# Optimization experiments

Measured on AMD Instinct MI355X. Metric: run time of the kernel, lower is better.

## Reference

```python
import jax, jax.numpy as jnp
import numpy as np
from functools import partial

T, B, I, H, L = 512, 256, 12, 256, 3


def setup_inputs() -> dict:
    key = jax.random.key(0)
    ks = jax.random.split(key, 1 + 4 * L + 2)
    inp = {"input": jax.random.normal(ks[0], (T, B, I), dtype=jnp.float32)}
    k = 1
    for l in range(L):
        in_dim = I if l == 0 else H
        s = 1.0 / np.sqrt(H)
        inp[f"w_ih{l}"] = jax.random.uniform(ks[k], (4 * H, in_dim), jnp.float32, -s, s); k += 1
        inp[f"w_hh{l}"] = jax.random.uniform(ks[k], (4 * H, H), jnp.float32, -s, s); k += 1
        inp[f"b_ih{l}"] = jax.random.uniform(ks[k], (4 * H,), jnp.float32, -s, s); k += 1
        inp[f"b_hh{l}"] = jax.random.uniform(ks[k], (4 * H,), jnp.float32, -s, s); k += 1
    s = 1.0 / np.sqrt(H)
    inp["w_lin"] = jax.random.uniform(ks[k], (1, H), jnp.float32, -s, s); k += 1
    inp["b_lin"] = jax.random.uniform(ks[k], (1,), jnp.float32, -s, s)
    return inp


def _lstm_layer(x, w_ih, w_hh, b_ih, b_hh):
    # x: (T, B, in_dim) -> hidden sequence (T, B, H)
    h_dim = w_hh.shape[1]
    xproj = jnp.einsum('tbi,gi->tbg', x, w_ih) + b_ih + b_hh  # (T, B, 4H)

    def step(carry, xp):
        h, c = carry
        gates = xp + h @ w_hh.T  # (B, 4H), torch gate order i,f,g,o
        i, f, g, o = jnp.split(gates, 4, axis=-1)
        i = jax.nn.sigmoid(i); f = jax.nn.sigmoid(f)
        g = jnp.tanh(g); o = jax.nn.sigmoid(o)
        c = f * c + i * g
        h = o * jnp.tanh(c)
        return (h, c), h

    bsz = x.shape[1]
    h0 = jnp.zeros((bsz, h_dim), x.dtype)
    c0 = jnp.zeros((bsz, h_dim), x.dtype)
    _, hs = jax.lax.scan(step, (h0, c0), xproj)
    return hs


def reference(input, w_ih0, w_hh0, b_ih0, b_hh0, w_ih1, w_hh1, b_ih1, b_hh1,
              w_ih2, w_hh2, b_ih2, b_hh2, w_lin, b_lin):
    params = [(w_ih0, w_hh0, b_ih0, b_hh0),
              (w_ih1, w_hh1, b_ih1, b_hh1),
              (w_ih2, w_hh2, b_ih2, b_hh2)]
    h = input
    for w_ih, w_hh, b_ih, b_hh in params:
        h = _lstm_layer(h, w_ih, w_hh, b_ih, b_hh)
    out = h @ w_lin.T + b_lin  # (T, B, 1)
    return out[..., 0]  # matches torch stack+squeeze -> (T, B)
```

## Files before the change

kernel.cpp:

```cpp
#include <hip/hip_runtime.h>

typedef _Float16 f16;
typedef _Float16 f16x4 __attribute__((ext_vector_type(4)));
typedef _Float16 f16x8 __attribute__((ext_vector_type(8)));
typedef float f32x4 __attribute__((ext_vector_type(4)));
typedef unsigned long long u64;

#define NSTEPS 512
#define NBATCH 256
#define HID 256
#define NL 3
#define NBG 8
#define NNW 8
#define ROWS 32
#define DRING 8
#define PITCH 260
#define THREADS 256
#define BKB 15
#define FLAGSTRIDE 16
#define NEG_INF_I (-2000000000)

#define WPACK_OFF ((size_t)65536)
#define WPACK_ELEMS ((size_t)64*16*64*8)
#define WPACK_SZB (WPACK_ELEMS*2)
#define RING_OFF (WPACK_OFF + 3*WPACK_SZB)
#define SLOT_Q 2048
#define RING_SZB ((size_t)NL*NBG*DRING*SLOT_Q*8)
#define WS_NEEDED (RING_OFF + RING_SZB)

__device__ __forceinline__ float sigm(float x){ return 1.f/(1.f+__expf(-x)); }
__device__ __forceinline__ float tanh_f(float x){ return 1.f - 2.f/(1.f+__expf(2.f*x)); }

__global__ __launch_bounds__(256) void pack_weights(
    const float* __restrict__ wih0, const float* __restrict__ whh0,
    const float* __restrict__ wih1, const float* __restrict__ whh1,
    const float* __restrict__ wih2, const float* __restrict__ whh2,
    unsigned char* __restrict__ ws)
{
  int gid = blockIdx.x*256 + threadIdx.x;
  if (gid >= 3*64*16*64) return;
  int lane  = gid & 63;
  int kb    = (gid>>6) & 15;
  int nt    = (gid>>10) & 63;
  int layer = gid>>16;
  const float* whh = (layer==0)?whh0:((layer==1)?whh1:whh2);
  const float* wih = (layer==0)?wih0:((layer==1)?wih1:wih2);
  int indim = (layer==0)?12:256;
  int n  = nt*16 + (lane&15);
  int k0 = kb*32 + (lane>>4)*8;
  f16x8 v;
  #pragma unroll
  for (int e=0;e<8;++e){
    int k = k0+e;
    float x;
    if (k < HID) x = whh[n*HID + k];
    else { int ki = k-HID; x = (ki<indim)? wih[n*indim+ki] : 0.f; }
    v[e] = (f16)x;
  }
  f16* dst = (f16*)(ws + WPACK_OFF) + (size_t)layer*WPACK_ELEMS
           + ((size_t)(nt*16+kb)*64 + lane)*8;
  *(f16x8*)dst = v;
}

template<int KB>
__device__ __forceinline__ void gates_mfma(
    const f16* __restrict__ Hown, const f16* __restrict__ Hin,
    const f16* __restrict__ BstL, const f16x8* __restrict__ b15,
    const float* __restrict__ bias,
    int wm, int wn, int lane, int c16, f32x4* acc)
{
  const int arow = wm*16 + c16;
  #pragma unroll
  for (int G=0;G<4;++G){ f32x4 z={bias[G],bias[G],bias[G],bias[G]}; acc[G]=z; }
  #pragma unroll
  for (int kb=0; kb<KB; ++kb){
    const f16* ap = (kb<8) ? &Hown[arow*PITCH + kb*32 + (lane>>4)*8]
                           : &Hin [arow*PITCH + (kb-8)*32 + (lane>>4)*8];
    f16x8 a = *(const f16x8*)ap;
    #pragma unroll
    for (int G=0; G<4; ++G){
      f16x8 b = (kb < BKB)
        ? ((const f16x8*)BstL)[ (size_t)((G*2+wn)*BKB + kb)*64 + lane ]
        : b15[G];
      acc[G] = __builtin_amdgcn_mfma_f32_16x16x32_f16(a, b, acc[G], 0,0,0);
    }
  }
}

__global__ __launch_bounds__(THREADS) void lstm_ws(
    const float* __restrict__ input,
    const float* __restrict__ bih0, const float* __restrict__ bhh0,
    const float* __restrict__ bih1, const float* __restrict__ bhh1,
    const float* __restrict__ bih2, const float* __restrict__ bhh2,
    const float* __restrict__ wlin, const float* __restrict__ blin,
    unsigned char* __restrict__ ws, float* __restrict__ out)
{
  __shared__ __attribute__((aligned(16))) f16 Bst[8*BKB*64*8];
  __shared__ __attribute__((aligned(16))) f16 Hown[ROWS*PITCH];
  __shared__ __attribute__((aligned(16))) f16 Hin [ROWS*PITCH];
  __shared__ float wlinLDS[HID];

  const int tid  = threadIdx.x;
  const int w    = tid >> 6;
  const int wm   = w >> 1, wn = w & 1;
  const int lane = tid & 63;
  const int c16  = lane & 15;
  const int r0   = (lane >> 4) * 4;
  const int bid  = blockIdx.x;
  const int bg   = bid & 7;
  const int nw   = (bid >> 3) & 7;
  const int layer= bid >> 6;
  const int rowsBase = bg * ROWS;
  const int unitBase = nw * 32;

  int* flags = (int*)ws;
  int* fOwn  = flags + (layer*NBG + bg)*32*FLAGSTRIDE;
  int* fLow  = (layer>0)? flags + ((layer-1)*NBG + bg)*32*FLAGSTRIDE : fOwn;
  int* fUp   = (layer<2)? flags + ((layer+1)*NBG + bg)*32*FLAGSTRIDE : fOwn;

  const f16* wp = (const f16*)(ws + WPACK_OFF) + (size_t)layer*WPACK_ELEMS;
  u64* ringSelfQ = (u64*)(ws + RING_OFF) + (size_t)((layer*NBG + bg)*DRING)*SLOT_Q;
  u64* ringLowQ  = (layer>0)? (u64*)(ws + RING_OFF) + (size_t)(((layer-1)*NBG + bg)*DRING)*SLOT_Q : (u64*)0;

  const f16x8* wpv = (const f16x8*)wp;
  f16x8* Bv = (f16x8*)Bst;
  #pragma unroll
  for (int nl=0; nl<8; ++nl){
    int G = nl>>1, s = nl&1;
    int nt = G*16 + nw*2 + s;
    for (int idx=tid; idx<BKB*64; idx+=THREADS)
      Bv[(size_t)nl*BKB*64 + idx] = wpv[(size_t)nt*1024 + idx];
  }
  f16x8 b15[4];
  #pragma unroll
  for (int G=0; G<4; ++G){
    int nt = G*16 + nw*2 + wn;
    b15[G] = wpv[(size_t)nt*1024 + 15*64 + lane];
  }
  if (tid < HID) wlinLDS[tid] = wlin[tid];

  const float* BIH = (layer==0)?bih0:((layer==1)?bih1:bih2);
  const float* BHH = (layer==0)?bhh0:((layer==1)?bhh1:bhh2);
  float bias[4], cst[4];
  const int unit = unitBase + wn*16 + c16;
  #pragma unroll
  for (int G=0;G<4;++G){
    int n = G*HID + unit;
    bias[G] = BIH[n] + BHH[n];
    cst[G] = 0.f;
  }
  const float bl = blin[0];
  const int rowblk = wm*4 + (r0>>2);

  for (int i=tid; i<ROWS*PITCH; i+=THREADS){ Hown[i]=(f16)0.f; Hin[i]=(f16)0.f; }
  __syncthreads();

  for (int t=0; t<NSTEPS; ++t){
    {
      const int which = lane >> 5, fidx = lane & 31;
      bool act = (which==0) || (layer>0);
      const int* p = (which==0)? fOwn + fidx*FLAGSTRIDE : fLow + fidx*FLAGSTRIDE;
      int need = act ? ((which==0)? t : t+1) : NEG_INF_I;
      int guard = 0;
      for(;;){
        int v = act ? __hip_atomic_load(p, __ATOMIC_RELAXED, __HIP_MEMORY_SCOPE_AGENT) : 0;
        if (__all(v >= need)) break;
        if (++guard > (1<<22)) break;
      }
    }
    if (layer<2 && (t&3)==0 && t>4){
      bool act = lane < 32;
      const int* p = fUp + (lane&31)*FLAGSTRIDE;
      int need = act ? t-4 : NEG_INF_I;
      int guard = 0;
      for(;;){
        int v = act ? __hip_atomic_load(p, __ATOMIC_RELAXED, __HIP_MEMORY_SCOPE_AGENT) : 0;
        if (__all(v >= need)) break;
        if (++guard > (1<<22)) break;
      }
    }
    asm volatile("" ::: "memory");

    u64 vown[8], vin[8];
    if (t > 0){
      const u64* src = ringSelfQ + (size_t)((t-1)&(DRING-1))*SLOT_Q;
      #pragma unroll
      for (int it=0; it<8; ++it)
        vown[it] = __hip_atomic_load(src + tid + it*THREADS,
                                     __ATOMIC_RELAXED, __HIP_MEMORY_SCOPE_AGENT);
    }
    if (layer > 0){
      const u64* src = ringLowQ + (size_t)(t&(DRING-1))*SLOT_Q;
      #pragma unroll
      for (int it=0; it<8; ++it)
        vin[it] = __hip_atomic_load(src + tid + it*THREADS,
                                    __ATOMIC_RELAXED, __HIP_MEMORY_SCOPE_AGENT);
    }
    if (t > 0){
      #pragma unroll
      for (int it=0; it<8; ++it){
        int i = tid + it*THREADS, rb = i>>8, un = i&255;
        union { u64 q; f16x4 h; } u; u.q = vown[it];
        f16* base = &Hown[(rb*4)*PITCH + un];
        base[0]=u.h[0]; base[PITCH]=u.h[1]; base[2*PITCH]=u.h[2]; base[3*PITCH]=u.h[3];
      }
    }
    if (layer > 0){
      #pragma unroll
      for (int it=0; it<8; ++it){
        int i = tid + it*THREADS, rb = i>>8, un = i&255;
        union { u64 q; f16x4 h; } u; u.q = vin[it];
        f16* base = &Hin[(rb*4)*PITCH + un];
        base[0]=u.h[0]; base[PITCH]=u.h[1]; base[2*PITCH]=u.h[2]; base[3*PITCH]=u.h[3];
      }
    } else {
      for (int idx=tid; idx<ROWS*12; idx+=THREADS){
        int r = idx/12, i = idx - r*12;
        Hin[r*PITCH + i] = (f16)input[((size_t)t*NBATCH + rowsBase + r)*12 + i];
      }
    }
    __syncthreads();

    f32x4 acc[4];
    if (layer==0) gates_mfma<9> (Hown, Hin, Bst, b15, bias, wm, wn, lane, c16, acc);
    else          gates_mfma<16>(Hown, Hin, Bst, b15, bias, wm, wn, lane, c16, acc);

    union { u64 q; f16x4 h; } hout;
    #pragma unroll
    for (int q=0;q<4;++q){
      float gi = sigm  (acc[0][q]);
      float gf = sigm  (acc[1][q]);
      float gg = tanh_f(acc[2][q]);
      float go = sigm  (acc[3][q]);
      float cv = gf*cst[q] + gi*gg; cst[q]=cv;
      hout.h[q] = (f16)(go*tanh_f(cv));
    }
    __hip_atomic_store(ringSelfQ + (size_t)(t&(DRING-1))*SLOT_Q + rowblk*256 + unit,
                       hout.q, __ATOMIC_RELAXED, __HIP_MEMORY_SCOPE_AGENT);
    asm volatile("s_waitcnt vmcnt(0)" ::: "memory");
    if (lane==0)
      __hip_atomic_store(fOwn + (nw*4 + w)*FLAGSTRIDE, t+1,
                         __ATOMIC_RELAXED, __HIP_MEMORY_SCOPE_AGENT);

    if (layer==2 && t>0){
      int row = tid>>3, kc = tid&7;
      float s = 0.f;
      #pragma unroll
      for (int cc=0; cc<4; ++cc){
        f16x8 hv = *(const f16x8*)&Hown[row*PITCH + kc*32 + cc*8];
        #pragma unroll
        for (int j=0;j<8;++j) s += (float)hv[j] * wlinLDS[kc*32 + cc*8 + j];
      }
      s += __shfl_xor(s,1); s += __shfl_xor(s,2); s += __shfl_xor(s,4);
      if (kc==0) out[(size_t)(t-1)*NBATCH + rowsBase + row] = s + bl;
    }
    __syncthreads();
  }

  if (layer==2){
    {
      bool act = lane < 32;
      const int* p = fOwn + (lane&31)*FLAGSTRIDE;
      int need = act ? NSTEPS : NEG_INF_I;
      int guard = 0;
      for(;;){
        int v = act ? __hip_atomic_load(p, __ATOMIC_RELAXED, __HIP_MEMORY_SCOPE_AGENT) : 0;
        if (__all(v >= need)) break;
        if (++guard > (1<<22)) break;
      }
    }
    asm volatile("" ::: "memory");
    const u64* src = ringSelfQ + (size_t)((NSTEPS-1)&(DRING-1))*SLOT_Q;
    #pragma unroll
    for (int it=0; it<8; ++it){
      int i = tid + it*THREADS, rb = i>>8, un = i&255;
      union { u64 q; f16x4 h; } u;
      u.q = __hip_atomic_load(src + i, __ATOMIC_RELAXED, __HIP_MEMORY_SCOPE_AGENT);
      f16* base = &Hown[(rb*4)*PITCH + un];
      base[0]=u.h[0]; base[PITCH]=u.h[1]; base[2*PITCH]=u.h[2]; base[3*PITCH]=u.h[3];
    }
    __syncthreads();
    int row = tid>>3, kc = tid&7;
    float s = 0.f;
    #pragma unroll
    for (int cc=0; cc<4; ++cc){
      f16x8 hv = *(const f16x8*)&Hown[row*PITCH + kc*32 + cc*8];
      #pragma unroll
      for (int j=0;j<8;++j) s += (float)hv[j] * wlinLDS[kc*32 + cc*8 + j];
    }
    s += __shfl_xor(s,1); s += __shfl_xor(s,2); s += __shfl_xor(s,4);
    if (kc==0) out[(size_t)(NSTEPS-1)*NBATCH + rowsBase + row] = s + bl;
  }
}

extern "C" void kernel_launch(void* const* d_in, const int* in_sizes, int n_in,
                              void* d_out, int out_size, void* d_ws, size_t ws_size,
                              hipStream_t stream)
{
  const float* input=(const float*)d_in[0];
  const float* wih0 =(const float*)d_in[1];
  const float* whh0 =(const float*)d_in[2];
  const float* bih0 =(const float*)d_in[3];
  const float* bhh0 =(const float*)d_in[4];
  const float* wih1 =(const float*)d_in[5];
  const float* whh1 =(const float*)d_in[6];
  const float* bih1 =(const float*)d_in[7];
  const float* bhh1 =(const float*)d_in[8];
  const float* wih2 =(const float*)d_in[9];
  const float* whh2 =(const float*)d_in[10];
  const float* bih2 =(const float*)d_in[11];
  const float* bhh2 =(const float*)d_in[12];
  const float* wlin =(const float*)d_in[13];
  const float* blin =(const float*)d_in[14];
  unsigned char* ws = (unsigned char*)d_ws;
  if (ws_size < WS_NEEDED) return;

  (void)hipMemsetAsync(ws, 0, WPACK_OFF, stream);
  hipLaunchKernelGGL(pack_weights, dim3(768), dim3(256), 0, stream,
                     wih0,whh0,wih1,whh1,wih2,whh2, ws);
  hipLaunchKernelGGL(lstm_ws, dim3(NL*NBG*NNW), dim3(THREADS), 0, stream,
                     input, bih0,bhh0,bih1,bhh1,bih2,bhh2, wlin, blin,
                     ws, (float*)d_out);
}
```

Measured before the change: 2.863 ms.

## Replace per-step flag polling with tagged ring slots carrying their timestep

Each ring entry now holds the f16x4 hidden values together with a timestep tag in a 16-byte granule. Consumers poll the data itself until every tag matches, so the separate per-wave progress flags, the store-then-waitcnt-then-flag handshake and the extra flag round trip each step go away. Upstream throttling now uses a coarser per-block progress counter updated every fourth step, and its spin loop sleeps between polls. This doubles ring traffic per step, adds a memset of the ring to 0xFF before each launch, and relies on 16-byte stores becoming visible atomically.

```diff
diff --git a/kernel.cpp b/kernel.cpp
--- a/kernel.cpp
+++ b/kernel.cpp
@@ -4,6 +4,7 @@
 typedef _Float16 f16x4 __attribute__((ext_vector_type(4)));
 typedef _Float16 f16x8 __attribute__((ext_vector_type(8)));
 typedef float f32x4 __attribute__((ext_vector_type(4)));
+typedef int i32x4 __attribute__((ext_vector_type(4)));
 typedef unsigned long long u64;
 
 #define NSTEPS 512
@@ -25,8 +26,10 @@
 #define WPACK_SZB (WPACK_ELEMS*2)
 #define RING_OFF (WPACK_OFF + 3*WPACK_SZB)
 #define SLOT_Q 2048
-#define RING_SZB ((size_t)NL*NBG*DRING*SLOT_Q*8)
+#define RING_SZB ((size_t)NL*NBG*DRING*SLOT_Q*16)
 #define WS_NEEDED (RING_OFF + RING_SZB)
+
+union Gran { i32x4 v; struct { f16x4 h; int tag; int pad; } s; };
 
 __device__ __forceinline__ float sigm(float x){ return 1.f/(1.f+__expf(-x)); }
 __device__ __forceinline__ float tanh_f(float x){ return 1.f - 2.f/(1.f+__expf(2.f*x)); }
@@ -114,13 +117,12 @@
   const int unitBase = nw * 32;
 
   int* flags = (int*)ws;
-  int* fOwn  = flags + (layer*NBG + bg)*32*FLAGSTRIDE;
-  int* fLow  = (layer>0)? flags + ((layer-1)*NBG + bg)*32*FLAGSTRIDE : fOwn;
-  int* fUp   = (layer<2)? flags + ((layer+1)*NBG + bg)*32*FLAGSTRIDE : fOwn;
+  int* progSelf = flags + (layer*NBG + bg)*8*FLAGSTRIDE;
+  int* progUp   = (layer<2)? flags + ((layer+1)*NBG + bg)*8*FLAGSTRIDE : progSelf;
 
   const f16* wp = (const f16*)(ws + WPACK_OFF) + (size_t)layer*WPACK_ELEMS;
-  u64* ringSelfQ = (u64*)(ws + RING_OFF) + (size_t)((layer*NBG + bg)*DRING)*SLOT_Q;
-  u64* ringLowQ  = (layer>0)? (u64*)(ws + RING_OFF) + (size_t)(((layer-1)*NBG + bg)*DRING)*SLOT_Q : (u64*)0;
+  i32x4* ringSelf = (i32x4*)(ws + RING_OFF) + (size_t)((layer*NBG + bg)*DRING)*SLOT_Q;
+  i32x4* ringLow  = (layer>0)? (i32x4*)(ws + RING_OFF) + (size_t)(((layer-1)*NBG + bg)*DRING)*SLOT_Q : (i32x4*)0;
 
   const f16x8* wpv = (const f16x8*)wp;
   f16x8* Bv = (f16x8*)Bst;
@@ -150,97 +152,109 @@
     cst[G] = 0.f;
   }
   const float bl = blin[0];
-  const int rowblk = wm*4 + (r0>>2);
+  const int rowblk = wm*4 + (lane>>4);
 
   for (int i=tid; i<ROWS*PITCH; i+=THREADS){ Hown[i]=(f16)0.f; Hin[i]=(f16)0.f; }
   __syncthreads();
 
   for (int t=0; t<NSTEPS; ++t){
-    {
-      const int which = lane >> 5, fidx = lane & 31;
-      bool act = (which==0) || (layer>0);
-      const int* p = (which==0)? fOwn + fidx*FLAGSTRIDE : fLow + fidx*FLAGSTRIDE;
-      int need = act ? ((which==0)? t : t+1) : NEG_INF_I;
-      int guard = 0;
-      for(;;){
-        int v = act ? __hip_atomic_load(p, __ATOMIC_RELAXED, __HIP_MEMORY_SCOPE_AGENT) : 0;
-        if (__all(v >= need)) break;
-        if (++guard > (1<<22)) break;
-      }
-    }
     if (layer<2 && (t&3)==0 && t>4){
-      bool act = lane < 32;
-      const int* p = fUp + (lane&31)*FLAGSTRIDE;
+      bool act = lane < 8;
+      const int* p = progUp + (lane&7)*FLAGSTRIDE;
       int need = act ? t-4 : NEG_INF_I;
       int guard = 0;
       for(;;){
         int v = act ? __hip_atomic_load(p, __ATOMIC_RELAXED, __HIP_MEMORY_SCOPE_AGENT) : 0;
         if (__all(v >= need)) break;
-        if (++guard > (1<<22)) break;
-      }
-    }
-    asm volatile("" ::: "memory");
-
-    u64 vown[8], vin[8];
-    if (t > 0){
-      const u64* src = ringSelfQ + (size_t)((t-1)&(DRING-1))*SLOT_Q;
-      #pragma unroll
-      for (int it=0; it<8; ++it)
-        vown[it] = __hip_atomic_load(src + tid + it*THREADS,
-                                     __ATOMIC_RELAXED, __HIP_MEMORY_SCOPE_AGENT);
-    }
-    if (layer > 0){
-      const u64* src = ringLowQ + (size_t)(t&(DRING-1))*SLOT_Q;
-      #pragma unroll
-      for (int it=0; it<8; ++it)
-        vin[it] = __hip_atomic_load(src + tid + it*THREADS,
-                                    __ATOMIC_RELAXED, __HIP_MEMORY_SCOPE_AGENT);
-    }
-    if (t > 0){
-      #pragma unroll
-      for (int it=0; it<8; ++it){
-        int i = tid + it*THREADS, rb = i>>8, un = i&255;
-        union { u64 q; f16x4 h; } u; u.q = vown[it];
-        f16* base = &Hown[(rb*4)*PITCH + un];
-        base[0]=u.h[0]; base[PITCH]=u.h[1]; base[2*PITCH]=u.h[2]; base[3*PITCH]=u.h[3];
-      }
-    }
-    if (layer > 0){
-      #pragma unroll
-      for (int it=0; it<8; ++it){
-        int i = tid + it*THREADS, rb = i>>8, un = i&255;
-        union { u64 q; f16x4 h; } u; u.q = vin[it];
-        f16* base = &Hin[(rb*4)*PITCH + un];
-        base[0]=u.h[0]; base[PITCH]=u.h[1]; base[2*PITCH]=u.h[2]; base[3*PITCH]=u.h[3];
-      }
-    } else {
+        if (++guard > (1<<18)) break;
+        __builtin_amdgcn_s_sleep(1);
+      }
+    }
+
+    if (layer == 0){
       for (int idx=tid; idx<ROWS*12; idx+=THREADS){
         int r = idx/12, i = idx - r*12;
         Hin[r*PITCH + i] = (f16)input[((size_t)t*NBATCH + rowsBase + r)*12 + i];
       }
     }
+
+    {
+      Gran go[8], gl[8];
+      const i32x4* srcO = ringSelf + (size_t)((t-1)&(DRING-1))*SLOT_Q + tid;
+      const i32x4* srcL = (layer>0)? ringLow + (size_t)(t&(DRING-1))*SLOT_Q + tid : (i32x4*)0;
+      const bool doOwn = (t>0), doLow = (layer>0);
+      int guard = 0;
+      for(;;){
+        if (doOwn){
+          #pragma unroll
+          for (int it=0; it<8; ++it)
+            asm volatile("global_load_dwordx4 %0, %1, off sc0 sc1"
+                         : "=v"(go[it].v) : "v"(srcO + it*THREADS) : "memory");
+        }
+        if (doLow){
+          #pragma unroll
+          for (int it=0; it<8; ++it)
+            asm volatile("global_load_dwordx4 %0, %1, off sc0 sc1"
+                         : "=v"(gl[it].v) : "v"(srcL + it*THREADS) : "memory");
+        }
+        asm volatile("s_waitcnt vmcnt(0)" ::: "memory");
+        __builtin_amdgcn_sched_barrier(0);
+        bool ok = true;
+        if (doOwn){
+          #pragma unroll
+          for (int it=0; it<8; ++it) ok = ok && (go[it].s.tag >= t-1);
+        }
+        if (doLow){
+          #pragma unroll
+          for (int it=0; it<8; ++it) ok = ok && (gl[it].s.tag >= t);
+        }
+        if (ok || ++guard > (1<<18)) break;
+      }
+      if (doOwn){
+        #pragma unroll
+        for (int it=0; it<8; ++it){
+          int i = tid + it*THREADS, rb = i>>8, un = i&255;
+          f16* base = &Hown[(rb*4)*PITCH + un];
+          base[0]=go[it].s.h[0]; base[PITCH]=go[it].s.h[1];
+          base[2*PITCH]=go[it].s.h[2]; base[3*PITCH]=go[it].s.h[3];
+        }
+      }
+      if (doLow){
+        #pragma unroll
+        for (int it=0; it<8; ++it){
+          int i = tid + it*THREADS, rb = i>>8, un = i&255;
+          f16* base = &Hin[(rb*4)*PITCH + un];
+          base[0]=gl[it].s.h[0]; base[PITCH]=gl[it].s.h[1];
+          base[2*PITCH]=gl[it].s.h[2]; base[3*PITCH]=gl[it].s.h[3];
+        }
+      }
+    }
     __syncthreads();
+
+    if (layer>0 && (t&3)==3 && tid==0)
+      __hip_atomic_store(progSelf + nw*FLAGSTRIDE, t+1,
+                         __ATOMIC_RELAXED, __HIP_MEMORY_SCOPE_AGENT);
 
     f32x4 acc[4];
     if (layer==0) gates_mfma<9> (Hown, Hin, Bst, b15, bias, wm, wn, lane, c16, acc);
     else          gates_mfma<16>(Hown, Hin, Bst, b15, bias, wm, wn, lane, c16, acc);
 
-    union { u64 q; f16x4 h; } hout;
+    Gran gg;
     #pragma unroll
     for (int q=0;q<4;++q){
       float gi = sigm  (acc[0][q]);
       float gf = sigm  (acc[1][q]);
-      float gg = tanh_f(acc[2][q]);
-      float go = sigm  (acc[3][q]);
-      float cv = gf*cst[q] + gi*gg; cst[q]=cv;
-      hout.h[q] = (f16)(go*tanh_f(cv));
-    }
-    __hip_atomic_store(ringSelfQ + (size_t)(t&(DRING-1))*SLOT_Q + rowblk*256 + unit,
-                       hout.q, __ATOMIC_RELAXED, __HIP_MEMORY_SCOPE_AGENT);
-    asm volatile("s_waitcnt vmcnt(0)" ::: "memory");
-    if (lane==0)
-      __hip_atomic_store(fOwn + (nw*4 + w)*FLAGSTRIDE, t+1,
-                         __ATOMIC_RELAXED, __HIP_MEMORY_SCOPE_AGENT);
+      float gg_ = tanh_f(acc[2][q]);
+      float go_ = sigm  (acc[3][q]);
+      float cv = gf*cst[q] + gi*gg_; cst[q]=cv;
+      gg.s.h[q] = (f16)(go_*tanh_f(cv));
+    }
+    gg.s.tag = t; gg.s.pad = 0;
+    {
+      i32x4* dst = ringSelf + (size_t)(t&(DRING-1))*SLOT_Q + rowblk*256 + unit;
+      asm volatile("global_store_dwordx4 %0, %1, off sc0 sc1"
+                   :: "v"(dst), "v"(gg.v) : "memory");
+    }
 
     if (layer==2 && t>0){
       int row = tid>>3, kc = tid&7;
@@ -258,26 +272,27 @@
   }
 
   if (layer==2){
-    {
-      bool act = lane < 32;
-      const int* p = fOwn + (lane&31)*FLAGSTRIDE;
-      int need = act ? NSTEPS : NEG_INF_I;
-      int guard = 0;
-      for(;;){
-        int v = act ? __hip_atomic_load(p, __ATOMIC_RELAXED, __HIP_MEMORY_SCOPE_AGENT) : 0;
-        if (__all(v >= need)) break;
-        if (++guard > (1<<22)) break;
-      }
-    }
-    asm volatile("" ::: "memory");
-    const u64* src = ringSelfQ + (size_t)((NSTEPS-1)&(DRING-1))*SLOT_Q;
+    Gran go[8];
+    const i32x4* srcO = ringSelf + (size_t)((NSTEPS-1)&(DRING-1))*SLOT_Q + tid;
+    int guard = 0;
+    for(;;){
+      #pragma unroll
+      for (int it=0; it<8; ++it)
+        asm volatile("global_load_dwordx4 %0, %1, off sc0 sc1"
+                     : "=v"(go[it].v) : "v"(srcO + it*THREADS) : "memory");
+      asm volatile("s_waitcnt vmcnt(0)" ::: "memory");
+      __builtin_amdgcn_sched_barrier(0);
+      bool ok = true;
+      #pragma unroll
+      for (int it=0; it<8; ++it) ok = ok && (go[it].s.tag >= NSTEPS-1);
+      if (ok || ++guard > (1<<18)) break;
+    }
     #pragma unroll
     for (int it=0; it<8; ++it){
       int i = tid + it*THREADS, rb = i>>8, un = i&255;
-      union { u64 q; f16x4 h; } u;
-      u.q = __hip_atomic_load(src + i, __ATOMIC_RELAXED, __HIP_MEMORY_SCOPE_AGENT);
       f16* base = &Hown[(rb*4)*PITCH + un];
-      base[0]=u.h[0]; base[PITCH]=u.h[1]; base[2*PITCH]=u.h[2]; base[3*PITCH]=u.h[3];
+      base[0]=go[it].s.h[0]; base[PITCH]=go[it].s.h[1];
+      base[2*PITCH]=go[it].s.h[2]; base[3*PITCH]=go[it].s.h[3];
     }
     __syncthreads();
     int row = tid>>3, kc = tid&7;
@@ -316,6 +331,7 @@
   if (ws_size < WS_NEEDED) return;
 
   (void)hipMemsetAsync(ws, 0, WPACK_OFF, stream);
+  (void)hipMemsetAsync(ws + RING_OFF, 0xFF, RING_SZB, stream);
   hipLaunchKernelGGL(pack_weights, dim3(768), dim3(256), 0, stream,
                      wih0,whh0,wih1,whh1,wih2,whh2, ws);
   hipLaunchKernelGGL(lstm_ws, dim3(NL*NBG*NNW), dim3(THREADS), 0, stream,
```

Measured after the change: 2.662 ms. 7.0% less time.
